# Optimization experiments

Hardware: AMD Instinct MI355X
Metric: run time of the kernel (lower is better)

The kernel has to match this reference:

```python
import jax, jax.numpy as jnp
import numpy as np

B, T, D = 2, 2048, 1024
HEADS, UNITS = 16, 64
OUT_DIM = 1024
_LARGE_BIAS = 10000.0


def _uniform(key, shape, fan_in, fan_out):
    limit = np.sqrt(6.0 / (fan_in + fan_out))
    return jax.random.uniform(key, shape, jnp.float32, -limit, limit)


def setup_inputs() -> dict:
    key = jax.random.key(0)
    kx, kq, kk, kv, ko = jax.random.split(key, 5)
    x = jax.random.normal(kx, (B, T, D), jnp.float32)
    mask = jnp.ones((B, T), jnp.int32)
    Wq = _uniform(kq, (D, HEADS * UNITS), D, UNITS)
    Wk = _uniform(kk, (D, HEADS * UNITS), D, UNITS)
    Wv = _uniform(kv, (D, HEADS * UNITS), D, UNITS)
    Wo = _uniform(ko, (HEADS * UNITS, OUT_DIM), HEADS * UNITS, OUT_DIM)
    return {"x": x, "mask": mask, "Wq": Wq, "Wk": Wk, "Wv": Wv, "Wo": Wo}


def reference(x, mask, Wq, Wk, Wv, Wo):
    m = mask.astype(x.dtype)                      # [B, T]
    x = x * m[:, :, None]                         # zero padded positions
    b, t, _ = x.shape
    # projections, split heads: [B, T, H, U]
    q = (x @ Wq).reshape(b, t, HEADS, UNITS)
    k = (x @ Wk).reshape(b, t, HEADS, UNITS)
    v = (x @ Wv).reshape(b, t, HEADS, UNITS)
    # logits[b,h,i,j] = sum_u q[b,i,h,u] k[b,j,h,u]
    logits = jnp.einsum('bihu,bjhu->bhij', q, k) / np.sqrt(UNITS).astype(x.dtype)
    # causal (forward) mask: subtract large bias above the diagonal
    causal = jnp.triu(jnp.full((t, t), _LARGE_BIAS, x.dtype), k=1)
    logits = logits - causal
    # padding mask on key axis
    logits = logits - ((1.0 - m) * _LARGE_BIAS)[:, None, None, :]
    weights = jax.nn.softmax(logits, axis=-1)     # [B, H, T, T]
    attended = jnp.einsum('bhij,bjhu->bihu', weights, v)
    attended = attended.reshape(b, t, HEADS * UNITS)
    return attended @ Wo                          # [B, T, OUT_DIM]
```

## Files before the change

kernel.cpp:

```cpp
#include <hip/hip_runtime.h>
#include <stdint.h>
#include <stddef.h>

#define B_ 2
#define T_ 2048
#define D_ 1024
#define H_ 16
#define U_ 64
#define M_ (B_ * T_)
#define N_ (H_ * U_)

typedef __attribute__((ext_vector_type(4))) float f32x4;
typedef __attribute__((ext_vector_type(8))) short s16x8;
typedef __attribute__((ext_vector_type(8))) __bf16 b16x8;

static_assert(sizeof(s16x8) == 16, "frag size");

__device__ __forceinline__ unsigned short f2bf(float f) {
  unsigned int u = __float_as_uint(f);
  u += 0x7FFFu + ((u >> 16) & 1u);
  return (unsigned short)(u >> 16);
}

__device__ __forceinline__ float exp2_hw(float x) {
  float r;
  asm("v_exp_f32 %0, %1" : "=v"(r) : "v"(x));
  return r;
}
__device__ __forceinline__ unsigned int cvtpk_bf16(float lo, float hi) {
  unsigned int r;
  asm("v_cvt_pk_bf16_f32 %0, %1, %2" : "=v"(r) : "v"(lo), "v"(hi));
  return r;
}

template <typename V>
__device__ __forceinline__ auto mfma16_impl(V a, V b, f32x4 c, int)
    -> decltype(__builtin_amdgcn_mfma_f32_16x16x32_bf16(a, b, c, 0, 0, 0)) {
  return __builtin_amdgcn_mfma_f32_16x16x32_bf16(a, b, c, 0, 0, 0);
}
template <typename V>
__device__ __forceinline__ f32x4 mfma16_impl(V a, V b, f32x4 c, long) {
  return __builtin_amdgcn_mfma_f32_16x16x32_bf16(
      __builtin_bit_cast(b16x8, a), __builtin_bit_cast(b16x8, b), c, 0, 0, 0);
}
__device__ __forceinline__ f32x4 mfma16(s16x8 a, s16x8 b, f32x4 c) {
  return mfma16_impl(a, b, c, 0);
}

__device__ __forceinline__ void gld16(const unsigned short* g, unsigned short* l) {
  __builtin_amdgcn_global_load_lds(
      (const __attribute__((address_space(1))) void*)g,
      (__attribute__((address_space(3))) void*)l, 16, 0, 0);
}

__global__ void prep_kernel(const float* __restrict__ x, const int* __restrict__ mask,
                            const float* __restrict__ w0, const float* __restrict__ w1,
                            const float* __restrict__ w2, const float* __restrict__ w3,
                            unsigned short* __restrict__ o0, unsigned short* __restrict__ o1,
                            unsigned short* __restrict__ o2, unsigned short* __restrict__ o3,
                            unsigned short* __restrict__ xb) {
  const int tid = threadIdx.x;
  if (blockIdx.x < 1024) {
    __shared__ float tile[64][68];
    const int id = blockIdx.x;
    const int mz = id >> 8, by = (id >> 4) & 15, bx = id & 15;
    const float* w;
    unsigned short* o;
    switch (mz) {
      case 0: w = w0; o = o0; break;
      case 1: w = w1; o = o1; break;
      case 2: w = w2; o = o2; break;
      default: w = w3; o = o3; break;
    }
    const int kb = by * 64, nb = bx * 64;
    const int r = tid >> 4, c4 = (tid & 15) * 4;
#pragma unroll
    for (int i = 0; i < 4; i++)
      *(float4*)&tile[r + i * 16][c4] =
          *(const float4*)(w + (size_t)(kb + r + i * 16) * 1024 + nb + c4);
    __syncthreads();
#pragma unroll
    for (int i = 0; i < 2; i++) {
      const int idx = tid + i * 256;
      const int n = idx >> 3;
      const int k0 = (idx & 7) * 8;
      unsigned int u0 = cvtpk_bf16(tile[k0 + 0][n], tile[k0 + 1][n]);
      unsigned int u1 = cvtpk_bf16(tile[k0 + 2][n], tile[k0 + 3][n]);
      unsigned int u2 = cvtpk_bf16(tile[k0 + 4][n], tile[k0 + 5][n]);
      unsigned int u3 = cvtpk_bf16(tile[k0 + 6][n], tile[k0 + 7][n]);
      uint4 o4 = {u0, u1, u2, u3};
      *(uint4*)(o + (size_t)(nb + n) * 1024 + kb + k0) = o4;
    }
  } else {
    const int idx = ((blockIdx.x - 1024) * 256 + tid) * 4;
    const int row = idx >> 10;
    const float m = (float)mask[row];
    float4 v = *(const float4*)(x + idx);
    ushort4 o;
    o.x = f2bf(v.x * m);
    o.y = f2bf(v.y * m);
    o.z = f2bf(v.z * m);
    o.w = f2bf(v.w * m);
    *(ushort4*)(xb + idx) = o;
  }
}

template <int MODE>
__device__ __forceinline__ void gemm64_body(const unsigned short* __restrict__ A,
                                            const unsigned short* __restrict__ Bt,
                                            void* __restrict__ Cout) {
  constexpr int Kd = 1024, Nd = 1024;
  __shared__ unsigned short la[128 * 64];
  __shared__ unsigned short lb[128 * 64];
  const int tid = threadIdx.x;
  const int lane = tid & 63;
  const int w = tid >> 6;
  const int mb = blockIdx.y * 128, nb = blockIdx.x * 128;
  const int wm = (w >> 1) * 64, wn = (w & 1) * 64;
  const int lr = lane & 15, lg = lane >> 4;
  const int srow = tid >> 3;
  const int scol = (tid & 7) * 8;
  const int sc = scol ^ ((srow & 7) << 3);
  const unsigned short* gA = A + (size_t)(mb + srow) * Kd + sc;
  const unsigned short* gB = Bt + (size_t)(nb + srow) * Kd + sc;
  unsigned short* lA = la + srow * 64 + scol;
  unsigned short* lB = lb + srow * 64 + scol;
  const int rsw = (lr & 7) << 3;

  f32x4 acc[4][4] = {};

  for (int kt = 0; kt < Kd; kt += 64) {
#pragma unroll
    for (int i = 0; i < 4; i++) {
      gld16(gA + kt + (size_t)(i * 32) * Kd, lA + i * 32 * 64);
      gld16(gB + kt + (size_t)(i * 32) * Kd, lB + i * 32 * 64);
    }
    __syncthreads();
#pragma unroll
    for (int ks = 0; ks < 2; ks++) {
      const int kc = (ks * 32 + lg * 8) ^ rsw;
      s16x8 af[4], bfr[4];
#pragma unroll
      for (int i = 0; i < 4; i++)
        af[i] = *(const s16x8*)(la + (wm + i * 16 + lr) * 64 + kc);
#pragma unroll
      for (int j = 0; j < 4; j++)
        bfr[j] = *(const s16x8*)(lb + (wn + j * 16 + lr) * 64 + kc);
#pragma unroll
      for (int i = 0; i < 4; i++)
#pragma unroll
        for (int j = 0; j < 4; j++)
          acc[i][j] = mfma16(af[i], bfr[j], acc[i][j]);
    }
    __syncthreads();
  }

#pragma unroll
  for (int i = 0; i < 4; i++)
#pragma unroll
    for (int j = 0; j < 4; j++) {
      const int col = nb + wn + j * 16 + lr;
      const int rowb = mb + wm + i * 16 + lg * 4;
      if (MODE == 0) {
        unsigned short* C = (unsigned short*)Cout;
#pragma unroll
        for (int r = 0; r < 4; r++) C[(size_t)(rowb + r) * Nd + col] = f2bf(acc[i][j][r]);
      } else {
        unsigned short* C = (unsigned short*)Cout;
        const size_t vrow = ((size_t)(rowb >> 11) * 16 + (col >> 6)) * 64 + (col & 63);
        ushort4 o;
#pragma unroll
        for (int r = 0; r < 4; r++) ((unsigned short*)&o)[r] = f2bf(acc[i][j][r]);
        *(ushort4*)(C + vrow * T_ + (rowb & 2047)) = o;
      }
    }
}

__global__ __launch_bounds__(256) void gemm_qkv(const unsigned short* __restrict__ A,
                                                const unsigned short* __restrict__ wq,
                                                const unsigned short* __restrict__ wk,
                                                const unsigned short* __restrict__ wv,
                                                unsigned short* __restrict__ cq,
                                                unsigned short* __restrict__ ck,
                                                unsigned short* __restrict__ vt) {
  if (blockIdx.z == 0) {
    gemm64_body<0>(A, wq, cq);
  } else if (blockIdx.z == 1) {
    gemm64_body<0>(A, wk, ck);
  } else {
    gemm64_body<2>(A, wv, vt);
  }
}

__global__ __launch_bounds__(256) void gemm_out(const unsigned short* __restrict__ A,
                                                const unsigned short* __restrict__ woT,
                                                float* __restrict__ C) {
  constexpr int Kd = 1024, Nd = 1024;
  __shared__ unsigned short la[128 * 64];
  __shared__ unsigned short lb[64 * 64];
  const int tid = threadIdx.x;
  const int lane = tid & 63;
  const int w = tid >> 6;
  const int mb = blockIdx.y * 128, nb = blockIdx.x * 64;
  const int wm = w * 32;
  const int lr = lane & 15, lg = lane >> 4;
  const int srow = tid >> 3;
  const int scol = (tid & 7) * 8;
  const int sc = scol ^ ((srow & 7) << 3);
  const unsigned short* gA = A + (size_t)(mb + srow) * Kd + sc;
  const unsigned short* gB = woT + (size_t)(nb + srow) * Kd + sc;
  unsigned short* lA = la + srow * 64 + scol;
  unsigned short* lB = lb + srow * 64 + scol;
  const int rsw = (lr & 7) << 3;

  f32x4 acc[2][4] = {};

  for (int kt = 0; kt < Kd; kt += 64) {
#pragma unroll
    for (int i = 0; i < 4; i++)
      gld16(gA + kt + (size_t)(i * 32) * Kd, lA + i * 32 * 64);
#pragma unroll
    for (int i = 0; i < 2; i++)
      gld16(gB + kt + (size_t)(i * 32) * Kd, lB + i * 32 * 64);
    __syncthreads();
#pragma unroll
    for (int ks = 0; ks < 2; ks++) {
      const int kc = (ks * 32 + lg * 8) ^ rsw;
      s16x8 af[2], bfr[4];
#pragma unroll
      for (int i = 0; i < 2; i++)
        af[i] = *(const s16x8*)(la + (wm + i * 16 + lr) * 64 + kc);
#pragma unroll
      for (int j = 0; j < 4; j++)
        bfr[j] = *(const s16x8*)(lb + (j * 16 + lr) * 64 + kc);
#pragma unroll
      for (int i = 0; i < 2; i++)
#pragma unroll
        for (int j = 0; j < 4; j++)
          acc[i][j] = mfma16(af[i], bfr[j], acc[i][j]);
    }
    __syncthreads();
  }

#pragma unroll
  for (int i = 0; i < 2; i++)
#pragma unroll
    for (int j = 0; j < 4; j++) {
      const int col = nb + j * 16 + lr;
      const int rowb = mb + wm + i * 16 + lg * 4;
#pragma unroll
      for (int r = 0; r < 4; r++) C[(size_t)(rowb + r) * Nd + col] = acc[i][j][r];
    }
}

__global__ __launch_bounds__(64) void attn17_kernel(const unsigned short* __restrict__ Q,
                                                    const unsigned short* __restrict__ K,
                                                    const unsigned short* __restrict__ Vt,
                                                    const int* __restrict__ mask,
                                                    unsigned short* __restrict__ att) {
  __shared__ unsigned short pbuf[32 * 64];
  const int lane = threadIdx.x & 63;
  const int li = lane & 15, lg = lane >> 4;
  const int bh = blockIdx.x & 31;
  const int b = bh >> 4, h = bh & 15;
  const int pr = blockIdx.x >> 5;

  const float CS = 0.125f * 1.44269504089f;
  const float PB = 10000.0f * 1.44269504089f;
  const float THR = 8.0f;

  const unsigned short* Kb = K + (size_t)(b * T_) * 1024 + h * 64;
  const unsigned short* Vtb = Vt + (size_t)bh * 64 * T_;
  const int* mk = mask + b * T_;

  const int xr = (li & 3) << 5;
  char* pbb = (char*)pbuf;

  for (int g = 0; g < 2; g++) {
    const int qg = g == 0 ? (63 - pr) : pr;
    const int q0 = qg * 32;

    s16x8 qf[2][2];
#pragma unroll
    for (int f = 0; f < 2; f++) {
      const unsigned short* qrow = Q + ((size_t)(b * T_) + q0 + f * 16 + li) * 1024 + h * 64;
      qf[f][0] = *(const s16x8*)(qrow + lg * 8);
      qf[f][1] = *(const s16x8*)(qrow + 32 + lg * 8);
    }

    const int iq0 = q0 + li, iq1 = q0 + 16 + li;

    float mrun[2] = {-1e30f, -1e30f};
    f32x4 lp[2] = {};
    f32x4 acc[4][2] = {};
    s16x8 vf[4][2];

    const int ntiles = (q0 + 95) >> 6;

    auto loadK = [&](s16x8 (&dst)[4][2], int jb) {
#pragma unroll
      for (int jf = 0; jf < 4; jf++) {
        const unsigned short* kr = Kb + (size_t)(jb + jf * 16 + li) * 1024 + lg * 8;
        dst[jf][0] = *(const s16x8*)kr;
        dst[jf][1] = *(const s16x8*)(kr + 32);
      }
    };
    auto loadM = [&](int4 (&dst)[4], int jb) {
#pragma unroll
      for (int jf = 0; jf < 4; jf++)
        dst[jf] = *(const int4*)(mk + jb + jf * 16 + lg * 4);
    };
    auto loadV = [&](int jb) {
#pragma unroll
      for (int uf = 0; uf < 4; uf++) {
        const unsigned short* vr = Vtb + (size_t)(uf * 16 + li) * T_ + jb + lg * 8;
        vf[uf][0] = *(const s16x8*)vr;
        vf[uf][1] = *(const s16x8*)(vr + 32);
      }
    };
    auto qk = [&](f32x4 (&s)[4][2], s16x8 (&kc)[4][2]) {
      __builtin_amdgcn_s_setprio(1);
#pragma unroll
      for (int jf = 0; jf < 4; jf++) {
        f32x4 z = {};
        s[jf][0] = mfma16(kc[jf][0], qf[0][0], z);
        s[jf][0] = mfma16(kc[jf][1], qf[0][1], s[jf][0]);
        f32x4 z2 = {};
        s[jf][1] = mfma16(kc[jf][0], qf[1][0], z2);
        s[jf][1] = mfma16(kc[jf][1], qf[1][1], s[jf][1]);
      }
      __builtin_amdgcn_s_setprio(0);
    };
    auto smw = [&](f32x4 (&s)[4][2], int4 (&mv)[4], int jb) {
      const bool diag = (jb + 64 > q0);
      const int band = (mv[0].x & mv[0].y & mv[0].z & mv[0].w) &
                       (mv[1].x & mv[1].y & mv[1].z & mv[1].w) &
                       (mv[2].x & mv[2].y & mv[2].z & mv[2].w) &
                       (mv[3].x & mv[3].y & mv[3].z & mv[3].w);
      const bool noBias = __all(band != 0);
#pragma unroll
      for (int f = 0; f < 2; f++) {
        const int iq = f ? iq1 : iq0;
        f32x4 pv4 = {-3e38f, -3e38f, -3e38f, -3e38f};
        if (noBias) {
#pragma unroll
          for (int jf = 0; jf < 4; jf++) {
            f32x4 zz = s[jf][f] * CS;
            if (diag) {
#pragma unroll
              for (int r = 0; r < 4; r++)
                if (jb + jf * 16 + lg * 4 + r > iq) zz[r] = -1e30f;
            }
            s[jf][f] = zz;
            pv4 = __builtin_elementwise_max(pv4, zz);
          }
        } else {
#pragma unroll
          for (int jf = 0; jf < 4; jf++) {
            f32x4 zz;
#pragma unroll
            for (int r = 0; r < 4; r++) {
              float z = fmaf(s[jf][f][r], CS, ((&mv[jf].x)[r] ? 0.f : -PB));
              if (diag && (jb + jf * 16 + lg * 4 + r > iq)) z = -1e30f;
              zz[r] = z;
            }
            s[jf][f] = zz;
            pv4 = __builtin_elementwise_max(pv4, zz);
          }
        }
        const float pmax = fmaxf(fmaxf(pv4[0], pv4[1]), fmaxf(pv4[2], pv4[3]));
        if (!__all(pmax <= mrun[f] + THR)) {
          float rmax = fmaxf(pmax, __shfl_xor(pmax, 16));
          rmax = fmaxf(rmax, __shfl_xor(rmax, 32));
          const float mnew = fmaxf(mrun[f], rmax);
          const float al = exp2_hw(mrun[f] - mnew);
          lp[f] *= al;
#pragma unroll
          for (int uf = 0; uf < 4; uf++) acc[uf][f] *= al;
          mrun[f] = mnew;
        }
        const float mm = mrun[f];
#pragma unroll
        for (int jf = 0; jf < 4; jf++) {
          f32x4 p;
#pragma unroll
          for (int r = 0; r < 4; r++) p[r] = exp2_hw(s[jf][f][r] - mm);
          lp[f] += p;
          uint2 w2;
          w2.x = cvtpk_bf16(p[0], p[1]);
          w2.y = cvtpk_bf16(p[2], p[3]);
          const int wb = (((f * 16 + li) * 64 + jf * 16 + lg * 4) * 2) ^ xr;
          *(uint2*)(pbb + wb) = w2;
        }
      }
    };
    auto pv = [&]() {
      s16x8 pfrag[2][2];
#pragma unroll
      for (int f = 0; f < 2; f++)
#pragma unroll
        for (int hh = 0; hh < 2; hh++) {
          const int rd = (((f * 16 + li) * 64 + hh * 32 + lg * 8) * 2) ^ xr;
          pfrag[f][hh] = *(const s16x8*)(pbb + rd);
        }
      __builtin_amdgcn_s_setprio(1);
#pragma unroll
      for (int uf = 0; uf < 4; uf++)
#pragma unroll
        for (int f = 0; f < 2; f++) {
          acc[uf][f] = mfma16(vf[uf][0], pfrag[f][0], acc[uf][f]);
          acc[uf][f] = mfma16(vf[uf][1], pfrag[f][1], acc[uf][f]);
        }
      __builtin_amdgcn_s_setprio(0);
    };

    s16x8 kA[4][2], kB[4][2];
    f32x4 sA[4][2], sB[4][2];
    int4 mA[4], mB[4];

    loadK(kA, 0);
    loadM(mA, 0);
    qk(sA, kA);
    if (ntiles > 1) {
      loadK(kB, 64);
      loadM(mB, 64);
    }

    int t = 0;
    while (true) {
      {
        const int jb = t * 64;
        loadV(jb);
        smw(sA, mA, jb);
        if (t + 1 < ntiles) qk(sB, kB);
        if (t + 2 < ntiles) {
          loadK(kA, (t + 2) * 64);
          loadM(mA, (t + 2) * 64);
        }
        pv();
      }
      if (t + 1 >= ntiles) break;
      {
        const int jb = (t + 1) * 64;
        loadV(jb);
        smw(sB, mB, jb);
        if (t + 2 < ntiles) qk(sA, kA);
        if (t + 3 < ntiles) {
          loadK(kB, (t + 3) * 64);
          loadM(mB, (t + 3) * 64);
        }
        pv();
      }
      t += 2;
      if (t >= ntiles) break;
    }

#pragma unroll
    for (int f = 0; f < 2; f++) {
      float l = (lp[f][0] + lp[f][1]) + (lp[f][2] + lp[f][3]);
      l += __shfl_xor(l, 16);
      l += __shfl_xor(l, 32);
      const float inv = 1.0f / l;
      unsigned short* arow = att + ((size_t)(b * T_) + q0 + f * 16 + li) * 1024 + h * 64;
#pragma unroll
      for (int uf = 0; uf < 4; uf++) {
        ushort4 o;
#pragma unroll
        for (int r = 0; r < 4; r++)
          ((unsigned short*)&o)[r] = __builtin_bit_cast(unsigned short, (__bf16)(acc[uf][f][r] * inv));
        *(ushort4*)(arow + uf * 16 + lg * 4) = o;
      }
    }
  }
}

extern "C" void kernel_launch(void* const* d_in, const int* in_sizes, int n_in,
                              void* d_out, int out_size, void* d_ws, size_t ws_size,
                              hipStream_t stream) {
  const float* x = (const float*)d_in[0];
  const int* mask = (const int*)d_in[1];
  const float* Wq = (const float*)d_in[2];
  const float* Wk = (const float*)d_in[3];
  const float* Wv = (const float*)d_in[4];
  const float* Wo = (const float*)d_in[5];

  const size_t MB = 1u << 20;
  char* ws = (char*)d_ws;
  unsigned short* wqT = (unsigned short*)(ws + 0 * MB);
  unsigned short* wkT = (unsigned short*)(ws + 2 * MB);
  unsigned short* wvT = (unsigned short*)(ws + 4 * MB);
  unsigned short* woT = (unsigned short*)(ws + 6 * MB);
  unsigned short* xb  = (unsigned short*)(ws + 8 * MB);
  unsigned short* qb  = (unsigned short*)(ws + 16 * MB);
  unsigned short* kb  = (unsigned short*)(ws + 24 * MB);
  unsigned short* vt  = (unsigned short*)(ws + 32 * MB);
  unsigned short* att = xb;
  (void)ws_size; (void)in_sizes; (void)n_in; (void)out_size;

  prep_kernel<<<dim3(5120), 256, 0, stream>>>(x, mask, Wq, Wk, Wv, Wo,
                                              wqT, wkT, wvT, woT, xb);
  gemm_qkv<<<dim3(8, 32, 3), 256, 0, stream>>>(xb, wqT, wkT, wvT, qb, kb, vt);
  attn17_kernel<<<dim3(1024), 64, 0, stream>>>(qb, kb, vt, mask, att);
  gemm_out<<<dim3(16, 32), 256, 0, stream>>>(att, woT, (float*)d_out);
}
```

Before: 137.3 us.

## Split attention KV tiles across two waves with flash-decoding style merge

The attention block now uses two wavefronts that interleave over key tiles (even and odd), each keeping its own running max, sum and accumulator. At the end, wave 1 writes its partial state to shared memory and wave 0 merges the two with rescaling before normalising and storing. This doubles the parallelism per query tile to hide latency and raise occupancy, at the cost of extra LDS traffic, two block barriers per query group and a merge step.

```diff
diff --git a/kernel.cpp b/kernel.cpp
--- a/kernel.cpp
+++ b/kernel.cpp
@@ -253,13 +253,15 @@
     }
 }
 
-__global__ __launch_bounds__(64) void attn17_kernel(const unsigned short* __restrict__ Q,
-                                                    const unsigned short* __restrict__ K,
-                                                    const unsigned short* __restrict__ Vt,
-                                                    const int* __restrict__ mask,
-                                                    unsigned short* __restrict__ att) {
-  __shared__ unsigned short pbuf[32 * 64];
-  const int lane = threadIdx.x & 63;
+__global__ __launch_bounds__(128) void attn19_kernel(const unsigned short* __restrict__ Q,
+                                                     const unsigned short* __restrict__ K,
+                                                     const unsigned short* __restrict__ Vt,
+                                                     const int* __restrict__ mask,
+                                                     unsigned short* __restrict__ att) {
+  __shared__ unsigned short pbuf[2][32 * 64];
+  __shared__ float cb[36 * 64];
+  const int tid = threadIdx.x;
+  const int w = tid >> 6, lane = tid & 63;
   const int li = lane & 15, lg = lane >> 4;
   const int bh = blockIdx.x & 31;
   const int b = bh >> 4, h = bh & 15;
@@ -274,7 +276,7 @@
   const int* mk = mask + b * T_;
 
   const int xr = (li & 3) << 5;
-  char* pbb = (char*)pbuf;
+  char* pbb = (char*)&pbuf[w][0];
 
   for (int g = 0; g < 2; g++) {
     const int qg = g == 0 ? (63 - pr) : pr;
@@ -296,6 +298,7 @@
     s16x8 vf[4][2];
 
     const int ntiles = (q0 + 95) >> 6;
+    const int nmy = (ntiles - w + 1) >> 1;
 
     auto loadK = [&](s16x8 (&dst)[4][2], int jb) {
 #pragma unroll
@@ -418,59 +421,90 @@
     f32x4 sA[4][2], sB[4][2];
     int4 mA[4], mB[4];
 
-    loadK(kA, 0);
-    loadM(mA, 0);
-    qk(sA, kA);
-    if (ntiles > 1) {
-      loadK(kB, 64);
-      loadM(mB, 64);
-    }
-
-    int t = 0;
-    while (true) {
-      {
-        const int jb = t * 64;
-        loadV(jb);
-        smw(sA, mA, jb);
-        if (t + 1 < ntiles) qk(sB, kB);
-        if (t + 2 < ntiles) {
-          loadK(kA, (t + 2) * 64);
-          loadM(mA, (t + 2) * 64);
-        }
-        pv();
-      }
-      if (t + 1 >= ntiles) break;
-      {
-        const int jb = (t + 1) * 64;
-        loadV(jb);
-        smw(sB, mB, jb);
-        if (t + 2 < ntiles) qk(sA, kA);
-        if (t + 3 < ntiles) {
-          loadK(kB, (t + 3) * 64);
-          loadM(mB, (t + 3) * 64);
-        }
-        pv();
-      }
-      t += 2;
-      if (t >= ntiles) break;
-    }
-
+    if (nmy > 0) {
+      loadK(kA, w * 64);
+      loadM(mA, w * 64);
+      qk(sA, kA);
+      if (nmy > 1) {
+        loadK(kB, (w + 2) * 64);
+        loadM(mB, (w + 2) * 64);
+      }
+      int i = 0;
+      while (true) {
+        {
+          const int jb = (w + 2 * i) * 64;
+          loadV(jb);
+          smw(sA, mA, jb);
+          if (i + 1 < nmy) qk(sB, kB);
+          if (i + 2 < nmy) {
+            loadK(kA, (w + 2 * (i + 2)) * 64);
+            loadM(mA, (w + 2 * (i + 2)) * 64);
+          }
+          pv();
+        }
+        if (i + 1 >= nmy) break;
+        {
+          const int jb = (w + 2 * (i + 1)) * 64;
+          loadV(jb);
+          smw(sB, mB, jb);
+          if (i + 2 < nmy) qk(sA, kA);
+          if (i + 3 < nmy) {
+            loadK(kB, (w + 2 * (i + 3)) * 64);
+            loadM(mB, (w + 2 * (i + 3)) * 64);
+          }
+          pv();
+        }
+        i += 2;
+        if (i >= nmy) break;
+      }
+    }
+
+    float lred[2];
 #pragma unroll
     for (int f = 0; f < 2; f++) {
       float l = (lp[f][0] + lp[f][1]) + (lp[f][2] + lp[f][3]);
       l += __shfl_xor(l, 16);
       l += __shfl_xor(l, 32);
-      const float inv = 1.0f / l;
-      unsigned short* arow = att + ((size_t)(b * T_) + q0 + f * 16 + li) * 1024 + h * 64;
-#pragma unroll
-      for (int uf = 0; uf < 4; uf++) {
-        ushort4 o;
-#pragma unroll
-        for (int r = 0; r < 4; r++)
-          ((unsigned short*)&o)[r] = __builtin_bit_cast(unsigned short, (__bf16)(acc[uf][f][r] * inv));
-        *(ushort4*)(arow + uf * 16 + lg * 4) = o;
-      }
-    }
+      lred[f] = l;
+    }
+    if (w == 1) {
+#pragma unroll
+      for (int f = 0; f < 2; f++)
+#pragma unroll
+        for (int uf = 0; uf < 4; uf++)
+#pragma unroll
+          for (int r = 0; r < 4; r++)
+            cb[(f * 16 + uf * 4 + r) * 64 + lane] = acc[uf][f][r];
+      cb[32 * 64 + lane] = mrun[0];
+      cb[33 * 64 + lane] = mrun[1];
+      cb[34 * 64 + lane] = lred[0];
+      cb[35 * 64 + lane] = lred[1];
+    }
+    __syncthreads();
+    if (w == 0) {
+#pragma unroll
+      for (int f = 0; f < 2; f++) {
+        const float mB2 = cb[(32 + f) * 64 + lane];
+        const float lB2 = cb[(34 + f) * 64 + lane];
+        const float m = fmaxf(mrun[f], mB2);
+        const float aA = exp2_hw(mrun[f] - m);
+        const float aB = exp2_hw(mB2 - m);
+        const float inv = 1.0f / (aA * lred[f] + aB * lB2);
+        unsigned short* arow = att + ((size_t)(b * T_) + q0 + f * 16 + li) * 1024 + h * 64;
+#pragma unroll
+        for (int uf = 0; uf < 4; uf++) {
+          ushort4 o;
+#pragma unroll
+          for (int r = 0; r < 4; r++) {
+            const float vB = cb[(f * 16 + uf * 4 + r) * 64 + lane];
+            const float v = (aA * acc[uf][f][r] + aB * vB) * inv;
+            ((unsigned short*)&o)[r] = __builtin_bit_cast(unsigned short, (__bf16)v);
+          }
+          *(ushort4*)(arow + uf * 16 + lg * 4) = o;
+        }
+      }
+    }
+    __syncthreads();
   }
 }
 
@@ -500,6 +534,6 @@
   prep_kernel<<<dim3(5120), 256, 0, stream>>>(x, mask, Wq, Wk, Wv, Wo,
                                               wqT, wkT, wvT, woT, xb);
   gemm_qkv<<<dim3(8, 32, 3), 256, 0, stream>>>(xb, wqT, wkT, wvT, qb, kb, vt);
-  attn17_kernel<<<dim3(1024), 64, 0, stream>>>(qb, kb, vt, mask, att);
+  attn19_kernel<<<dim3(1024), 128, 0, stream>>>(qb, kb, vt, mask, att);
   gemm_out<<<dim3(16, 32), 256, 0, stream>>>(att, woT, (float*)d_out);
 }
```

New measurement: 145.2 us. +5.7%, slower.
